# Kernel optimization log

Hardware: AMD Instinct MI355X
Metric: run time of the kernel (lower is better)

Reference implementation:

```python
import jax, jax.numpy as jnp
import numpy as np
import math

B, S, D, H = 8, 512, 1024, 16
HD = D // H  # 64
FF = 4 * D
EPS = 1e-5


def setup_inputs() -> dict:
    key = jax.random.key(0)
    ks = jax.random.split(key, 12)
    sc = 0.02
    return {
        "x":   jax.random.normal(ks[0], (B, S, D), jnp.float32),
        "Wq":  jax.random.normal(ks[1], (H, D, HD), jnp.float32) * sc,
        "Wk":  jax.random.normal(ks[2], (H, D, HD), jnp.float32) * sc,
        "Wv":  jax.random.normal(ks[3], (H, D, HD), jnp.float32) * sc,
        "Wo":  jax.random.normal(ks[4], (D, D), jnp.float32) * sc,
        "bo":  jnp.zeros((D,), jnp.float32),
        "g1":  jnp.ones((D,), jnp.float32),
        "b1":  jnp.zeros((D,), jnp.float32),
        "g2":  jnp.ones((D,), jnp.float32),
        "b2":  jnp.zeros((D,), jnp.float32),
        "W1":  jax.random.normal(ks[5], (D, FF), jnp.float32) * sc,
        "bf1": jnp.zeros((FF,), jnp.float32),
        "W2":  jax.random.normal(ks[6], (FF, D), jnp.float32) * sc,
        "bf2": jnp.zeros((D,), jnp.float32),
    }


def _layernorm(x, gamma, beta):
    # biased variance, matches torch.var(correction=0)
    mean = jnp.mean(x, axis=-1, keepdims=True)
    var = jnp.mean((x - mean) ** 2, axis=-1, keepdims=True)
    return (x - mean) / jnp.sqrt(var + EPS) * gamma + beta


def _block(x, Wq, Wk, Wv, Wo, bo, g1, b1, g2, b2, W1, bf1, W2, bf2):
    h = _layernorm(x, g1, b1)
    # per-head projections (no bias): [B,H,S,HD]
    Q = jnp.einsum("bsd,hde->bhse", h, Wq)
    K = jnp.einsum("bsd,hde->bhse", h, Wk)
    V = jnp.einsum("bsd,hde->bhse", h, Wv)
    scores = jnp.einsum("bhse,bhte->bhst", Q, K) / math.sqrt(HD)
    causal = jnp.triu(jnp.ones((S, S), bool), k=1)  # upper-triangular masked
    scores = jnp.where(causal, jnp.float32(-1e10), scores)
    att = jax.nn.softmax(scores, axis=-1)  # dropout in eval mode = identity
    ctx = jnp.einsum("bhst,bhte->bhse", att, V)
    # concat heads in order -> [B,S,D]
    ctx = ctx.transpose(0, 2, 1, 3).reshape(B, S, D)
    attn_out = ctx @ Wo + bo
    cache = attn_out + x
    h2 = _layernorm(cache, g2, b2)
    ff = jax.nn.gelu(h2 @ W1 + bf1, approximate=False) @ W2 + bf2
    return ff + cache


def reference(x, Wq, Wk, Wv, Wo, bo, g1, b1, g2, b2, W1, bf1, W2, bf2):
    return _block(x, Wq, Wk, Wv, Wo, bo, g1, b1, g2, b2, W1, bf1, W2, bf2)
```

## Files before the change

kernel.cpp:

```cpp
#include <hip/hip_runtime.h>
#include <hip/hip_bf16.h>

typedef __hip_bfloat16 bf16;

#define B_   8
#define S_   512
#define D_   1024
#define H_   16
#define HD_  64
#define FF_  4096
#define ROWS (B_ * S_)

typedef __attribute__((ext_vector_type(8))) unsigned short u16x8;
typedef __attribute__((ext_vector_type(4))) float f32x4;

typedef __attribute__((address_space(1))) const unsigned int GU32;
typedef __attribute__((address_space(3))) unsigned int LU32;
__device__ __forceinline__ void gld16(const void* g, void* l) {
    __builtin_amdgcn_global_load_lds((GU32*)g, (LU32*)l, 16, 0, 0);
}

__device__ __forceinline__ float bf2f(unsigned short u) {
    union { unsigned int i; float f; } v; v.i = ((unsigned int)u) << 16; return v.f;
}
__device__ __forceinline__ unsigned short f2bfu(float f) {
    bf16 h = __float2bfloat16(f);
    return *reinterpret_cast<unsigned short*>(&h);
}
__device__ __forceinline__ float ldsel(const void* p, size_t i, bool f32) {
    return f32 ? ((const float*)p)[i]
               : __bfloat162float(((const bf16*)p)[i]);
}
__device__ __forceinline__ float gelu_exact(float x) {
    return 0.5f * x * (1.f + erff(x * 0.70710678118654752440f));
}

__global__ __launch_bounds__(256) void ln_kernel(const void* __restrict__ x,
                                                 const void* __restrict__ gam,
                                                 const void* __restrict__ bet,
                                                 bf16* __restrict__ out,
                                                 int x_ws,
                                                 const unsigned short* __restrict__ probe) {
    bool pf32 = (probe[0] == 0);
    bool xf32 = (!x_ws) && pf32;
    int row = blockIdx.x;
    int tid = threadIdx.x;
    size_t rb = (size_t)row * D_;
    float v[4];
#pragma unroll
    for (int i = 0; i < 4; ++i) v[i] = ldsel(x, rb + tid + i * 256, xf32);
    float s  = v[0] + v[1] + v[2] + v[3];
    float s2 = v[0] * v[0] + v[1] * v[1] + v[2] * v[2] + v[3] * v[3];
#pragma unroll
    for (int off = 32; off > 0; off >>= 1) {
        s  += __shfl_down(s, off);
        s2 += __shfl_down(s2, off);
    }
    __shared__ float red[8];
    int wv = tid >> 6, ln = tid & 63;
    if (ln == 0) { red[wv] = s; red[4 + wv] = s2; }
    __syncthreads();
    s  = red[0] + red[1] + red[2] + red[3];
    s2 = red[4] + red[5] + red[6] + red[7];
    float mean = s * (1.f / 1024.f);
    float var  = s2 * (1.f / 1024.f) - mean * mean;
    float rstd = rsqrtf(var + 1e-5f);
#pragma unroll
    for (int i = 0; i < 4; ++i) {
        int c = tid + i * 256;
        float g = ldsel(gam, c, pf32), b = ldsel(bet, c, pf32);
        out[rb + c] = __float2bfloat16((v[i] - mean) * rstd * g + b);
    }
}

__global__ __launch_bounds__(256) void transpose_kernel(
    const void* __restrict__ src, bf16* __restrict__ dst,
    int N, int K, int sK, int sH,
    const unsigned short* __restrict__ probe) {
    bool pf32 = (probe[0] == 0);
    int tilesN = N >> 6;
    int tn = blockIdx.x % tilesN, tk = blockIdx.x / tilesN;
    int n0 = tn * 64, k0 = tk * 64;
    __shared__ float T[64][65];
    int t = threadIdx.x;
    size_t headoff = (size_t)(n0 >> 6) * sH;
#pragma unroll
    for (int i = 0; i < 16; ++i) {
        int lin = t + i * 256;
        int kl = lin >> 6, nl = lin & 63;
        size_t e = headoff + (size_t)(k0 + kl) * sK + nl;
        T[kl][nl] = ldsel(src, e, pf32);
    }
    __syncthreads();
#pragma unroll
    for (int i = 0; i < 16; ++i) {
        int lin = t + i * 256;
        int nl = lin >> 6, kl = lin & 63;
        dst[(size_t)(n0 + nl) * K + k0 + kl] = __float2bfloat16(T[kl][nl]);
    }
}

template<int BN>
__global__ __launch_bounds__(256) void gemm_mfma(
    const bf16* __restrict__ A, const bf16* __restrict__ Bt,
    int K, int nSeg, int segShift, size_t segStride,
    const void* __restrict__ bias,
    const void* __restrict__ resid, int resid_ws,
    bf16* __restrict__ outWS, void* __restrict__ outFinal, int mode,
    const unsigned short* __restrict__ probe) {
    constexpr int BM  = 128;
    constexpr int NR  = BN / 32;
    constexpr int CH  = 8 + BN / 16;
    constexpr int NCH = CH / 4;
    bool pf32 = (probe[0] == 0);
    __shared__ alignas(16) unsigned short As[2][BM * 32];
    __shared__ alignas(16) unsigned short Bs[2][BN * 32];
    int tid  = threadIdx.x;
    int lane = tid & 63, wv = tid >> 6;
    int g = lane >> 4, i16 = lane & 15;
    int wrow = wv >> 1, wcol = wv & 1;

    int GX = gridDim.x;
    int total = GX * gridDim.y;
    int bid = blockIdx.y * GX + blockIdx.x;
    int swz = bid;
    if ((total & 7) == 0) swz = (bid & 7) * (total >> 3) + (bid >> 3);
    int m0 = (swz / GX) * BM, n0 = (swz % GX) * BN;

    f32x4 acc[4][NR];
#pragma unroll
    for (int i = 0; i < 4; ++i)
#pragma unroll
        for (int j = 0; j < NR; ++j) acc[i][j] = (f32x4){0.f, 0.f, 0.f, 0.f};

    const unsigned short* gsrc[NCH];
    unsigned short* l0[NCH];
    unsigned short* l1[NCH];
    {
        int rl = lane >> 2, kq = (lane & 3) * 8;
#pragma unroll
        for (int c0 = 0; c0 < NCH; ++c0) {
            int c = c0 * 4 + wv;
            if (c < 8) {
                gsrc[c0] = (const unsigned short*)A + (size_t)(m0 + c * 16 + rl) * K + kq;
                l0[c0] = &As[0][c * 512];
                l1[c0] = &As[1][c * 512];
            } else {
                gsrc[c0] = (const unsigned short*)Bt + (size_t)(n0 + (c - 8) * 16 + rl) * K + kq;
                l0[c0] = &Bs[0][(c - 8) * 512];
                l1[c0] = &Bs[1][(c - 8) * 512];
            }
        }
    }

#define STAGE0(KOFF) { _Pragma("unroll") \
    for (int c0 = 0; c0 < NCH; ++c0) gld16(gsrc[c0] + (KOFF), l0[c0]); }
#define STAGE1(KOFF) { _Pragma("unroll") \
    for (int c0 = 0; c0 < NCH; ++c0) gld16(gsrc[c0] + (KOFF), l1[c0]); }
#define COMPUTE(BUF) { \
    u16x8 af[4], bfv[NR]; \
    _Pragma("unroll") \
    for (int i = 0; i < 4; ++i) \
        af[i] = *reinterpret_cast<const u16x8*>(&As[BUF][(wrow * 64 + i * 16 + i16) * 32 + g * 8]); \
    _Pragma("unroll") \
    for (int j = 0; j < NR; ++j) \
        bfv[j] = *reinterpret_cast<const u16x8*>(&Bs[BUF][(wcol * (BN / 2) + j * 16 + i16) * 32 + g * 8]); \
    _Pragma("unroll") \
    for (int i = 0; i < 4; ++i) \
        _Pragma("unroll") \
        for (int j = 0; j < NR; ++j) \
            asm("v_mfma_f32_16x16x32_bf16 %0, %1, %2, %0" \
                : "+v"(acc[i][j]) : "v"(af[i]), "v"(bfv[j])); }

    STAGE0(0);
    __syncthreads();
    for (int k0 = 0; k0 < K; k0 += 64) {
        STAGE1(k0 + 32);
        COMPUTE(0);
        __syncthreads();
        if (k0 + 64 < K) STAGE0(k0 + 64);
        COMPUTE(1);
        __syncthreads();
    }
#undef STAGE0
#undef STAGE1
#undef COMPUTE

    __builtin_amdgcn_sched_barrier(0);
    asm volatile("s_nop 7\n\ts_nop 7\n\ts_nop 7" ::: );
    __builtin_amdgcn_sched_barrier(0);

    int coll = i16, rowl = g * 4;
#pragma unroll
    for (int j = 0; j < NR; ++j) {
        int n = n0 + wcol * (BN / 2) + j * 16 + coll;
        int seg = n >> segShift;
        int nl = n & (nSeg - 1);
        float bval = (mode != 0) ? ldsel(bias, nl, pf32) : 0.f;
        bf16* ows = outWS + (size_t)seg * segStride;
#pragma unroll
        for (int i = 0; i < 4; ++i) {
            int mb = m0 + wrow * 64 + i * 16 + rowl;
#pragma unroll
            for (int r = 0; r < 4; ++r) {
                size_t idx = (size_t)(mb + r) * nSeg + nl;
                float c = acc[i][j][r];
                if (mode == 1) {
                    c += bval;
                    c += resid_ws ? __bfloat162float(((const bf16*)resid)[idx])
                                  : ldsel(resid, idx, pf32);
                } else if (mode == 2) {
                    c = gelu_exact(c + bval);
                }
                if (outFinal) {
                    if (pf32) ((float*)outFinal)[idx] = c;
                    else      ((bf16*)outFinal)[idx] = __float2bfloat16(c);
                } else {
                    ows[idx] = __float2bfloat16(c);
                }
            }
        }
    }
}

__global__ __launch_bounds__(256) void attn_kernel(const bf16* __restrict__ Qg,
                                                   const bf16* __restrict__ Kg,
                                                   const bf16* __restrict__ Vg,
                                                   bf16* __restrict__ Og) {
    constexpr int P = 72;
    __shared__ alignas(16) unsigned short Ks[64 * P];
    __shared__ alignas(16) unsigned short Vt[64 * P];
    __shared__ alignas(16) unsigned short Ps[64 * P];
    int qb = blockIdx.x;
    int bh = blockIdx.y;
    int b = bh >> 4, h = bh & 15;
    int tid = threadIdx.x;
    int lane = tid & 63, wv = tid >> 6;
    int g = lane >> 4, i16 = lane & 15;
    size_t base = ((size_t)b * S_) * D_ + h * HD_;

    u16x8 qa[2];
    {
        const unsigned short* qp = (const unsigned short*)Qg + base
            + (size_t)(qb * 64 + wv * 16 + i16) * D_ + g * 8;
#pragma unroll
        for (int kk = 0; kk < 2; ++kk) {
            u16x8 v = *reinterpret_cast<const u16x8*>(qp + kk * 32);
#pragma unroll
            for (int e = 0; e < 8; ++e) v[e] = f2bfu(bf2f(v[e]) * 0.125f);
            qa[kk] = v;
        }
    }
    f32x4 ov[4];
#pragma unroll
    for (int dj = 0; dj < 4; ++dj) ov[dj] = (f32x4){0.f, 0.f, 0.f, 0.f};
    float mrow[4], lrow[4];
#pragma unroll
    for (int r = 0; r < 4; ++r) { mrow[r] = -1e30f; lrow[r] = 0.f; }

    int st = tid >> 2, sd = (tid & 3) * 16;
    const unsigned short* Kp = (const unsigned short*)Kg + base + (size_t)st * D_ + sd;
    const unsigned short* Vp = (const unsigned short*)Vg + base + (size_t)st * D_ + sd;
    unsigned short* KsW = &Ks[st * P + sd];
    unsigned short* VtW = &Vt[sd * P + (st ^ sd)];
    int g1 = g >> 1, g0 = g & 1;
    unsigned short* PsW = &Ps[(wv * 16 + g * 4) * P + (i16 ^ (g0 << 3))];
    const unsigned short* PsR = &Ps[(wv * 16 + i16) * P + ((g ^ ((i16 >> 2) & 3)) << 3)];

    for (int kb = 0; kb <= qb; ++kb) {
        __syncthreads();
        size_t ko = (size_t)kb * 64 * D_;
        u16x8 k0 = *reinterpret_cast<const u16x8*>(Kp + ko);
        u16x8 k1 = *reinterpret_cast<const u16x8*>(Kp + ko + 8);
        u16x8 v0 = *reinterpret_cast<const u16x8*>(Vp + ko);
        u16x8 v1 = *reinterpret_cast<const u16x8*>(Vp + ko + 8);
        *reinterpret_cast<u16x8*>(KsW)     = k0;
        *reinterpret_cast<u16x8*>(KsW + 8) = k1;
#pragma unroll
        for (int ii = 0; ii < 8; ++ii) VtW[ii * P] = v0[ii];
#pragma unroll
        for (int ii = 0; ii < 8; ++ii) VtW[(ii + 8) * P] = v1[ii];
        __syncthreads();

        f32x4 sc[4];
#pragma unroll
        for (int tj = 0; tj < 4; ++tj) sc[tj] = (f32x4){0.f, 0.f, 0.f, 0.f};
#pragma unroll
        for (int kk = 0; kk < 2; ++kk)
#pragma unroll
            for (int tj = 0; tj < 4; ++tj) {
                u16x8 kf = *reinterpret_cast<const u16x8*>(
                    &Ks[(tj * 16 + i16) * P + kk * 32 + g * 8]);
                asm("v_mfma_f32_16x16x32_bf16 %0, %1, %2, %0"
                    : "+v"(sc[tj]) : "v"(qa[kk]), "v"(kf));
            }
        __builtin_amdgcn_sched_barrier(0);
        asm volatile("s_nop 7\n\ts_nop 7\n\ts_nop 7" ::: );
        __builtin_amdgcn_sched_barrier(0);

        if (kb == qb) {
#pragma unroll
            for (int tj = 0; tj < 4; ++tj)
#pragma unroll
                for (int r = 0; r < 4; ++r)
                    if (tj * 16 + i16 > wv * 16 + g * 4 + r) sc[tj][r] = -1e30f;
        }
        float al[4];
#pragma unroll
        for (int r = 0; r < 4; ++r) {
            float mt = fmaxf(fmaxf(sc[0][r], sc[1][r]), fmaxf(sc[2][r], sc[3][r]));
            mt = fmaxf(mt, __shfl_xor(mt, 1));
            mt = fmaxf(mt, __shfl_xor(mt, 2));
            mt = fmaxf(mt, __shfl_xor(mt, 4));
            mt = fmaxf(mt, __shfl_xor(mt, 8));
            float mnew = fmaxf(mrow[r], mt);
            al[r] = __expf(mrow[r] - mnew);
            mrow[r] = mnew;
        }
        float psum[4] = {0.f, 0.f, 0.f, 0.f};
        unsigned short pw[4][4];
#pragma unroll
        for (int tj = 0; tj < 4; ++tj)
#pragma unroll
            for (int r = 0; r < 4; ++r) {
                float p = __expf(sc[tj][r] - mrow[r]);
                unsigned short pb = f2bfu(p);
                pw[tj][r] = pb;
                psum[r] += bf2f(pb);
            }
#pragma unroll
        for (int r = 0; r < 4; ++r) {
            float ps = psum[r];
            ps += __shfl_xor(ps, 1);
            ps += __shfl_xor(ps, 2);
            ps += __shfl_xor(ps, 4);
            ps += __shfl_xor(ps, 8);
            lrow[r] = lrow[r] * al[r] + ps;
        }
#pragma unroll
        for (int dj = 0; dj < 4; ++dj)
#pragma unroll
            for (int r = 0; r < 4; ++r) ov[dj][r] *= al[r];
#pragma unroll
        for (int r = 0; r < 4; ++r)
#pragma unroll
            for (int tj = 0; tj < 4; ++tj)
                PsW[r * P + ((tj ^ g1) << 4)] = pw[tj][r];
#pragma unroll
        for (int kk = 0; kk < 2; ++kk) {
            u16x8 pf = *reinterpret_cast<const u16x8*>(PsR + kk * 32);
#pragma unroll
            for (int dj = 0; dj < 4; ++dj) {
                int tcol = ((kk << 5) | (g << 3)) ^ (dj << 4);
                u16x8 vf = *reinterpret_cast<const u16x8*>(
                    &Vt[(dj * 16 + i16) * P + tcol]);
                asm("v_mfma_f32_16x16x32_bf16 %0, %1, %2, %0"
                    : "+v"(ov[dj]) : "v"(pf), "v"(vf));
            }
        }
    }
    __builtin_amdgcn_sched_barrier(0);
    asm volatile("s_nop 7\n\ts_nop 7\n\ts_nop 7" ::: );
    __builtin_amdgcn_sched_barrier(0);
    float rl[4];
#pragma unroll
    for (int r = 0; r < 4; ++r) rl[r] = 1.f / lrow[r];
    bf16* op = Og + base + (size_t)(qb * 64 + wv * 16 + g * 4) * D_ + i16;
#pragma unroll
    for (int r = 0; r < 4; ++r)
#pragma unroll
        for (int dj = 0; dj < 4; ++dj)
            op[(size_t)r * D_ + dj * 16] = __float2bfloat16(ov[dj][r] * rl[r]);
}

extern "C" void kernel_launch(void* const* d_in, const int* in_sizes, int n_in,
                              void* d_out, int out_size, void* d_ws, size_t ws_size,
                              hipStream_t stream) {
    const void* x   = d_in[0];
    const void* Wq  = d_in[1];
    const void* Wk  = d_in[2];
    const void* Wv  = d_in[3];
    const void* Wo  = d_in[4];
    const void* bo  = d_in[5];
    const void* g1  = d_in[6];
    const void* b1  = d_in[7];
    const void* g2  = d_in[8];
    const void* b2  = d_in[9];
    const void* W1  = d_in[10];
    const void* bf1 = d_in[11];
    const void* W2  = d_in[12];
    const void* bf2 = d_in[13];
    const unsigned short* probe = (const unsigned short*)g1;

    bf16* ws = (bf16*)d_ws;
    const size_t Mi = (size_t)1024 * 1024;
    bf16* h     = ws;
    bf16* Qb    = ws + 4 * Mi;
    bf16* Kb    = ws + 8 * Mi;
    bf16* Vb    = ws + 12 * Mi;
    bf16* ctx   = ws;
    bf16* cache = ws + 4 * Mi;
    bf16* h2    = ws + 8 * Mi;
    bf16* ff1   = ws + 12 * Mi;
    bf16* WqT   = ws + 16 * Mi;
    bf16* WkT   = ws + 17 * Mi;
    bf16* WvT   = ws + 18 * Mi;
    bf16* WoT   = ws + 19 * Mi;
    bf16* W1T   = ws;
    bf16* W2T   = ws + 8 * Mi;

    transpose_kernel<<<256, 256, 0, stream>>>(Wq, WqT, 1024, 1024, HD_, D_ * HD_, probe);
    transpose_kernel<<<256, 256, 0, stream>>>(Wk, WkT, 1024, 1024, HD_, D_ * HD_, probe);
    transpose_kernel<<<256, 256, 0, stream>>>(Wv, WvT, 1024, 1024, HD_, D_ * HD_, probe);
    transpose_kernel<<<256, 256, 0, stream>>>(Wo, WoT, 1024, 1024, 1024, 64, probe);
    ln_kernel<<<ROWS, 256, 0, stream>>>(x, g1, b1, h, 0, probe);
    gemm_mfma<128><<<dim3(3072 / 128, ROWS / 128), 256, 0, stream>>>(
        h, WqT, 1024, 1024, 10, 4 * Mi,
        nullptr, nullptr, 0, Qb, nullptr, 0, probe);
    dim3 gA(S_ / 64, B_ * H_);
    attn_kernel<<<gA, 256, 0, stream>>>(Qb, Kb, Vb, ctx);
    gemm_mfma<64><<<dim3(1024 / 64, ROWS / 128), 256, 0, stream>>>(
        ctx, WoT, 1024, 1024, 30, 0,
        bo, x, 0, cache, nullptr, 1, probe);
    transpose_kernel<<<1024, 256, 0, stream>>>(W1, W1T, 4096, 1024, FF_, 64, probe);
    ln_kernel<<<ROWS, 256, 0, stream>>>(cache, g2, b2, h2, 1, probe);
    gemm_mfma<128><<<dim3(4096 / 128, ROWS / 128), 256, 0, stream>>>(
        h2, W1T, 1024, 4096, 30, 0,
        bf1, nullptr, 0, ff1, nullptr, 2, probe);
    transpose_kernel<<<1024, 256, 0, stream>>>(W2, W2T, 1024, 4096, 1024, 64, probe);
    gemm_mfma<64><<<dim3(1024 / 64, ROWS / 128), 256, 0, stream>>>(
        ff1, W2T, 4096, 1024, 30, 0,
        bf2, cache, 1, nullptr, d_out, 1, probe);
}
```

Measured before the change: 430.4 us.

## Deepen GEMM LDS pipeline to four stages with vmcnt-based waits

Replaces the double-buffered LDS pipeline in the MFMA GEMM with a 4-buffer ring that keeps three k-slices of global->LDS loads in flight. Explicit s_waitcnt vmcnt counts and raw s_barrier replace __syncthreads, and s_setprio raises wave priority around the MFMA block. The goal is to hide global load latency better. In exchange LDS use doubles, which may reduce occupancy, and the hand-tuned wait counts and the single barrier per stage must stay correct for reuse of each buffer.

```diff
diff --git a/kernel.cpp b/kernel.cpp
--- a/kernel.cpp
+++ b/kernel.cpp
@@ -113,8 +113,8 @@
     constexpr int CH  = 8 + BN / 16;
     constexpr int NCH = CH / 4;
     bool pf32 = (probe[0] == 0);
-    __shared__ alignas(16) unsigned short As[2][BM * 32];
-    __shared__ alignas(16) unsigned short Bs[2][BN * 32];
+    __shared__ alignas(16) unsigned short As[4][BM * 32];
+    __shared__ alignas(16) unsigned short Bs[4][BN * 32];
     int tid  = threadIdx.x;
     int lane = tid & 63, wv = tid >> 6;
     int g = lane >> 4, i16 = lane & 15;
@@ -134,8 +134,7 @@
         for (int j = 0; j < NR; ++j) acc[i][j] = (f32x4){0.f, 0.f, 0.f, 0.f};
 
     const unsigned short* gsrc[NCH];
-    unsigned short* l0[NCH];
-    unsigned short* l1[NCH];
+    unsigned short* ldst[4][NCH];
     {
         int rl = lane >> 2, kq = (lane & 3) * 8;
 #pragma unroll
@@ -143,20 +142,24 @@
             int c = c0 * 4 + wv;
             if (c < 8) {
                 gsrc[c0] = (const unsigned short*)A + (size_t)(m0 + c * 16 + rl) * K + kq;
-                l0[c0] = &As[0][c * 512];
-                l1[c0] = &As[1][c * 512];
+#pragma unroll
+                for (int bb = 0; bb < 4; ++bb) ldst[bb][c0] = &As[bb][c * 512];
             } else {
                 gsrc[c0] = (const unsigned short*)Bt + (size_t)(n0 + (c - 8) * 16 + rl) * K + kq;
-                l0[c0] = &Bs[0][(c - 8) * 512];
-                l1[c0] = &Bs[1][(c - 8) * 512];
+#pragma unroll
+                for (int bb = 0; bb < 4; ++bb) ldst[bb][c0] = &Bs[bb][(c - 8) * 512];
             }
         }
     }
 
-#define STAGE0(KOFF) { _Pragma("unroll") \
-    for (int c0 = 0; c0 < NCH; ++c0) gld16(gsrc[c0] + (KOFF), l0[c0]); }
-#define STAGE1(KOFF) { _Pragma("unroll") \
-    for (int c0 = 0; c0 < NCH; ++c0) gld16(gsrc[c0] + (KOFF), l1[c0]); }
+#define STAGE(BUF, KOFF) { _Pragma("unroll") \
+    for (int c0 = 0; c0 < NCH; ++c0) gld16(gsrc[c0] + (KOFF), ldst[BUF][c0]); }
+#define WAITV2N { if constexpr (NCH == 3) asm volatile("s_waitcnt vmcnt(6)" ::: "memory"); \
+                  else                    asm volatile("s_waitcnt vmcnt(8)" ::: "memory"); }
+#define WAITV1N { if constexpr (NCH == 3) asm volatile("s_waitcnt vmcnt(3)" ::: "memory"); \
+                  else                    asm volatile("s_waitcnt vmcnt(4)" ::: "memory"); }
+#define WAITV0  asm volatile("s_waitcnt vmcnt(0)" ::: "memory")
+#define BARR { __builtin_amdgcn_s_barrier(); __builtin_amdgcn_sched_barrier(0); }
 #define COMPUTE(BUF) { \
     u16x8 af[4], bfv[NR]; \
     _Pragma("unroll") \
@@ -165,25 +168,34 @@
     _Pragma("unroll") \
     for (int j = 0; j < NR; ++j) \
         bfv[j] = *reinterpret_cast<const u16x8*>(&Bs[BUF][(wcol * (BN / 2) + j * 16 + i16) * 32 + g * 8]); \
+    __builtin_amdgcn_s_setprio(1); \
     _Pragma("unroll") \
     for (int i = 0; i < 4; ++i) \
         _Pragma("unroll") \
         for (int j = 0; j < NR; ++j) \
             asm("v_mfma_f32_16x16x32_bf16 %0, %1, %2, %0" \
-                : "+v"(acc[i][j]) : "v"(af[i]), "v"(bfv[j])); }
-
-    STAGE0(0);
-    __syncthreads();
-    for (int k0 = 0; k0 < K; k0 += 64) {
-        STAGE1(k0 + 32);
-        COMPUTE(0);
-        __syncthreads();
-        if (k0 + 64 < K) STAGE0(k0 + 64);
-        COMPUTE(1);
-        __syncthreads();
-    }
-#undef STAGE0
-#undef STAGE1
+                : "+v"(acc[i][j]) : "v"(af[i]), "v"(bfv[j])); \
+    __builtin_amdgcn_s_setprio(0); }
+
+    STAGE(0, 0); STAGE(1, 32); STAGE(2, 64);
+    for (int k0 = 0; k0 + 256 <= K; k0 += 128) {
+        WAITV2N; BARR; STAGE(3, k0 + 96);  COMPUTE(0);
+        WAITV2N; BARR; STAGE(0, k0 + 128); COMPUTE(1);
+        WAITV2N; BARR; STAGE(1, k0 + 160); COMPUTE(2);
+        WAITV2N; BARR; STAGE(2, k0 + 192); COMPUTE(3);
+    }
+    {
+        int k0 = K - 128;
+        WAITV2N; BARR; STAGE(3, k0 + 96); COMPUTE(0);
+        WAITV2N; BARR; COMPUTE(1);
+        WAITV1N; BARR; COMPUTE(2);
+        WAITV0;  BARR; COMPUTE(3);
+    }
+#undef STAGE
+#undef WAITV2N
+#undef WAITV1N
+#undef WAITV0
+#undef BARR
 #undef COMPUTE
 
     __builtin_amdgcn_sched_barrier(0);
```

Measured after the change: 456.6 us. 6.1% more time.
